# Kernel tuning notes

Measured on AMD Instinct MI355X. Metric: run time of the kernel, lower is better.

## Reference

```python
import jax, jax.numpy as jnp
import numpy as np
from jax import lax

SPARSITY = 0.5  # args.sparsity: fraction of weights KEPT


def get_subnet(scores, k):
    """GetSubnet.forward: sort |scores|, zero lowest (1-k) fraction, one elsewhere."""
    sa = jnp.abs(scores)
    n = sa.size
    j = int((1.0 - k) * n)  # static: number of entries zeroed
    idx = jnp.argsort(sa.ravel())  # ascending, matches torch .sort()
    mask = jnp.zeros((n,), dtype=sa.dtype).at[idx[j:]].set(1.0)
    return mask.reshape(scores.shape)


def masked_conv(x, w, s, b, stride):
    m = get_subnet(s, SPARSITY)
    y = lax.conv_general_dilated(
        x, w * m, window_strides=(stride, stride), padding=((1, 1), (1, 1)),
        dimension_numbers=('NCHW', 'OIHW', 'NCHW'))
    return y + b[None, :, None, None]


def setup_inputs() -> dict:
    key = jax.random.key(0)
    ks = jax.random.split(key, 16)
    def rn(k, shape, scale):
        return jax.random.normal(k, shape, dtype=jnp.float32) * scale
    return {
        'x':   rn(ks[0], (64, 3, 64, 64), 1.0),
        'w1':  rn(ks[1], (128, 3, 3, 3), 0.2),   's1': rn(ks[2], (128, 3, 3, 3), 1.0),   'b1': rn(ks[3], (128,), 0.01),
        'w2':  rn(ks[4], (256, 128, 3, 3), 0.05), 's2': rn(ks[5], (256, 128, 3, 3), 1.0), 'b2': rn(ks[6], (256,), 0.01),
        'w3':  rn(ks[7], (512, 256, 3, 3), 0.03), 's3': rn(ks[8], (512, 256, 3, 3), 1.0), 'b3': rn(ks[9], (512,), 0.01),
        'fw1': rn(ks[10], (1024, 512), 0.05),     'fs1': rn(ks[11], (1024, 512), 1.0),    'fb1': rn(ks[12], (1024,), 0.01),
        'fw2': rn(ks[13], (10, 1024), 0.05),      'fs2': rn(ks[14], (10, 1024), 1.0),     'fb2': rn(ks[15], (10,), 0.01),
    }


def reference(x, w1, s1, b1, w2, s2, b2, w3, s3, b3, fw1, fs1, fb1, fw2, fs2, fb2):
    h = jax.nn.relu(masked_conv(x, w1, s1, b1, stride=1))   # [64,128,64,64]
    h = jax.nn.relu(masked_conv(h, w2, s2, b2, stride=2))   # [64,256,32,32]
    h = jax.nn.relu(masked_conv(h, w3, s3, b3, stride=2))   # [64,512,16,16]
    h = h.mean(axis=(2, 3))                                 # [64,512] global avg pool
    m1 = get_subnet(fs1, SPARSITY)
    h = jax.nn.relu(h @ (fw1 * m1).T + fb1)                 # [64,1024]
    m2 = get_subnet(fs2, SPARSITY)
    return h @ (fw2 * m2).T + fb2                           # [64,10]
```

## Files before the change

### kernel.cpp

```cpp
#include <hip/hip_runtime.h>
#include <stdint.h>


typedef __attribute__((ext_vector_type(8))) short short8;
typedef __attribute__((ext_vector_type(4))) short short4v;
typedef __attribute__((ext_vector_type(4))) float floatx4;

__device__ __forceinline__ unsigned short f2bf(float f) {
    unsigned u = __float_as_uint(f);
    u += 0x7fffu + ((u >> 16) & 1u);
    return (unsigned short)(u >> 16);
}

__device__ __forceinline__ void stage16(const unsigned short* g, unsigned short* l) {
    __builtin_amdgcn_global_load_lds(
        (const __attribute__((address_space(1))) unsigned int*)(const void*)g,
        (__attribute__((address_space(3))) unsigned int*)(void*)l,
        16, 0, 0);
}

constexpr unsigned CUM0 = 3456u;
constexpr unsigned CUM1 = 298368u;
constexpr unsigned CUM2 = 1478016u;
constexpr unsigned CUM3 = 2002304u;
constexpr unsigned STOT = 2012544u;
constexpr int NBH = 512;

__device__ __forceinline__ int find_tensor(unsigned idx, unsigned& li) {
    if (idx < CUM0) { li = idx;        return 0; }
    if (idx < CUM1) { li = idx - CUM0; return 1; }
    if (idx < CUM2) { li = idx - CUM1; return 2; }
    if (idx < CUM3) { li = idx - CUM2; return 3; }
    li = idx - CUM3; return 4;
}

__global__ __launch_bounds__(256) void hist11(const float* __restrict__ s0,
                                              const float* __restrict__ s1,
                                              const float* __restrict__ s2,
                                              const float* __restrict__ s3,
                                              const float* __restrict__ s4,
                                              const unsigned* __restrict__ P,
                                              unsigned* __restrict__ ghist, int pass) {
    __shared__ unsigned lh[10240];
    const int tid = threadIdx.x;
    const int NB = (pass == 2) ? 512 : 2048;
    for (int i = tid; i < NB * 5; i += 256) lh[i] = 0;
    __syncthreads();

    unsigned pref[5];
    #pragma unroll
    for (int t = 0; t < 5; t++) pref[t] = pass ? P[t] : 0u;
    const int fsh = (pass == 1) ? 20 : 9;

    for (unsigned idx = blockIdx.x * 256u + tid; idx < STOT; idx += NBH * 256u) {
        unsigned li; int t = find_tensor(idx, li);
        const float* sp = t == 0 ? s0 : t == 1 ? s1 : t == 2 ? s2 : t == 3 ? s3 : s4;
        unsigned key = __float_as_uint(sp[li]) & 0x7fffffffu;
        bool ok = (pass == 0) || ((key >> fsh) == pref[t]);
        if (ok) {
            unsigned bin = (pass == 0) ? (key >> 20)
                         : (pass == 1) ? ((key >> 9) & 2047u)
                                       : (key & 511u);
            atomicAdd(&lh[(unsigned)t * NB + bin], 1u);
        }
    }
    __syncthreads();
    const int goff = (pass == 0) ? 0 : (pass == 1) ? 10240 : 20480;
    for (int i = tid; i < NB * 5; i += 256) {
        unsigned v = lh[i];
        if (v) atomicAdd(&ghist[goff + i], v);
    }
}

__global__ __launch_bounds__(256) void find11(const unsigned* __restrict__ ghist,
                                              unsigned* __restrict__ P,
                                              unsigned* __restrict__ targ, int pass) {
    const int t = blockIdx.x;
    const int tid = threadIdx.x;
    const int NB = (pass == 2) ? 512 : 2048;
    const int goff = (pass == 0) ? 0 : (pass == 1) ? 10240 : 20480;
    const int seg = NB / 256;
    __shared__ unsigned bins[2048];
    __shared__ unsigned part[256];
    for (int i = tid; i < NB; i += 256) bins[i] = ghist[goff + t * NB + i];
    __syncthreads();
    unsigned s = 0;
    for (int j = 0; j < seg; j++) s += bins[tid * seg + j];
    part[tid] = s;
    __syncthreads();
    if (tid == 0) {
        unsigned n = t == 0 ? 3456u : t == 1 ? 294912u : t == 2 ? 1179648u
                   : t == 3 ? 524288u : 10240u;
        unsigned target = (pass == 0) ? (n >> 1) : targ[t];
        unsigned cum = 0; int q = 0;
        for (; q < 256; q++) { unsigned c = part[q]; if (cum + c > target) break; cum += c; }
        int b = q * seg;
        for (;; b++) { unsigned c = bins[b]; if (cum + c > target) break; cum += c; }
        targ[t] = target - cum;
        if (pass == 0)      P[t] = (unsigned)b;
        else if (pass == 1) P[t] = (P[t] << 11) | (unsigned)b;
        else                P[t] = (P[t] << 9) | (unsigned)b;
    }
}

__global__ void mask_reorder(const float* __restrict__ w0, const float* __restrict__ w1,
                             const float* __restrict__ w2, const float* __restrict__ w3,
                             const float* __restrict__ w4,
                             const float* __restrict__ s0, const float* __restrict__ s1,
                             const float* __restrict__ s2, const float* __restrict__ s3,
                             const float* __restrict__ s4,
                             const unsigned* __restrict__ T,
                             float* __restrict__ wm1,
                             unsigned short* __restrict__ A2,
                             unsigned short* __restrict__ A3,
                             float* __restrict__ fwm1, float* __restrict__ fwm2,
                             float* __restrict__ pooled) {
    unsigned idx = blockIdx.x * 256u + threadIdx.x;
    if (idx >= STOT) return;
    if (idx < 32768u) pooled[idx] = 0.f;
    unsigned li; int t = find_tensor(idx, li);
    const float* sp = t == 0 ? s0 : t == 1 ? s1 : t == 2 ? s2 : t == 3 ? s3 : s4;
    const float* wp = t == 0 ? w0 : t == 1 ? w1 : t == 2 ? w2 : t == 3 ? w3 : w4;
    unsigned key = __float_as_uint(sp[li]) & 0x7fffffffu;
    float val = (key >= T[t]) ? wp[li] : 0.f;
    if (t == 0) {
        wm1[li] = val;
    } else if (t == 1) {
        unsigned k = li / 1152u, r = li - k * 1152u;
        unsigned c = r / 9u, e = r - c * 9u;
        A2[((size_t)e * 256u + k) * 128u + c] = f2bf(val);
    } else if (t == 2) {
        unsigned k = li / 2304u, r = li - k * 2304u;
        unsigned c = r / 9u, e = r - c * 9u;
        A3[((size_t)e * 512u + k) * 256u + c] = f2bf(val);
    } else if (t == 3) {
        fwm1[li] = val;
    } else {
        fwm2[li] = val;
    }
}

template <int C, int H, int W, int K, int TX, int TY, int KT>
__global__ __launch_bounds__(TX* TY) void conv_direct(const float* __restrict__ in,
                                                      const float* __restrict__ wm,
                                                      const float* __restrict__ bias,
                                                      unsigned short* __restrict__ out) {
    constexpr int TILW = TX * 2, TILH = TY * 2;
    constexpr int ITW = TILW + 2, ITH = TILH + 2;
    constexpr int NTHREADS = TX * TY;
    constexpr int NLOAD = (ITH * ITW + NTHREADS - 1) / NTHREADS;
    constexpr int KG = K / KT;

    __shared__ float sIn[ITH * ITW];
    __shared__ float sW[9 * KT];

    const int tid = threadIdx.x;
    const int tx = tid % TX, ty = tid / TX;
    const int kg = blockIdx.z % KG, n = blockIdx.z / KG;
    const int ox0 = blockIdx.x * TILW, oy0 = blockIdx.y * TILH;
    const int ix0 = ox0 - 1, iy0 = oy0 - 1;

    const float* inN = in + (size_t)n * C * H * W;
    const float* wkg = wm + (size_t)kg * KT * C * 9;

    int goff[NLOAD];
    #pragma unroll
    for (int i = 0; i < NLOAD; i++) {
        int idx = tid + i * NTHREADS;
        if (idx < ITH * ITW) {
            int r = idx / ITW, col = idx % ITW;
            int gy = iy0 + r, gx = ix0 + col;
            goff[i] = (gy >= 0 && gy < H && gx >= 0 && gx < W) ? (gy * W + gx) : -1;
        } else goff[i] = -2;
    }

    float acc[2][2][KT];
    #pragma unroll
    for (int py = 0; py < 2; py++)
        #pragma unroll
        for (int px = 0; px < 2; px++)
            #pragma unroll
            for (int j = 0; j < KT; j++) acc[py][px][j] = 0.f;

    for (int c = 0; c < C; c++) {
        const float* inC = inN + (size_t)c * H * W;
        #pragma unroll
        for (int i = 0; i < NLOAD; i++) {
            int g = goff[i];
            if (g >= -1) sIn[tid + i * NTHREADS] = (g >= 0) ? inC[g] : 0.f;
        }
        for (int i = tid; i < 9 * KT; i += NTHREADS) {
            int e = i / KT, j = i % KT;
            sW[i] = wkg[j * C * 9 + c * 9 + e];
        }
        __syncthreads();

        float vin[4][4];
        const float* base = &sIn[(ty * 2) * ITW + tx * 2];
        #pragma unroll
        for (int r = 0; r < 4; r++)
            #pragma unroll
            for (int cc = 0; cc < 4; cc++) vin[r][cc] = base[r * ITW + cc];

        #pragma unroll
        for (int e = 0; e < 9; e++) {
            const int dy = e / 3, dx = e % 3;
            #pragma unroll
            for (int j = 0; j < KT; j++) {
                float wv = sW[e * KT + j];
                #pragma unroll
                for (int py = 0; py < 2; py++)
                    #pragma unroll
                    for (int px = 0; px < 2; px++)
                        acc[py][px][j] = fmaf(vin[py + dy][px + dx], wv, acc[py][px][j]);
            }
        }
        __syncthreads();
    }

    float bj[KT];
    #pragma unroll
    for (int j = 0; j < KT; j++) bj[j] = bias[kg * KT + j];
    #pragma unroll
    for (int py = 0; py < 2; py++)
        #pragma unroll
        for (int px = 0; px < 2; px++) {
            int oy = oy0 + ty * 2 + py, ox = ox0 + tx * 2 + px;
            short8 v;
            #pragma unroll
            for (int j = 0; j < KT; j++) {
                float t = acc[py][px][j] + bj[j];
                v[j] = (short)f2bf(t > 0.f ? t : 0.f);
            }
            *(short8*)(out + ((size_t)(n * H + oy) * W + ox) * K + kg * KT) = v;
        }
}

template <int C, int H, int W, int KOUT, int NPIX, bool POOL, bool SWAPYZ>
__global__ __launch_bounds__(256, 3) void conv_mfma(const unsigned short* __restrict__ in,
                                                    const unsigned short* __restrict__ A,
                                                    const float* __restrict__ bias,
                                                    const unsigned short* __restrict__ zg,
                                                    void* __restrict__ outv) {
    constexpr int OH = H / 2, OW = W / 2;
    constexpr int PR = NPIX / OW;
    constexpr int FN = NPIX / 16;
    constexpr int RH = 2 * PR + 1;
    constexpr int IW = W + 1;
    constexpr int NC = C / 32;
    constexpr int NPT = RH * IW;
    constexpr int NPTP = (NPT + 7) & ~7;
    constexpr int NSLOT = 4 * NPTP;
    constexpr int SLMAX = (NSLOT + 255) / 256;
    constexpr int SLOTS_PAD = SLMAX * 256;

    __shared__ unsigned short sIn[2][SLOTS_PAD * 8];

    const int tid = threadIdx.x;
    const int lane = tid & 63;
    const int wv = tid >> 6;
    const int l15 = lane & 15;
    const int quad = lane >> 4;
    const int pt = blockIdx.x;
    const int kb = SWAPYZ ? blockIdx.z : blockIdx.y;
    const int n  = SWAPYZ ? blockIdx.y : blockIdx.z;
    const int k0 = kb * 128;
    const int oy0 = pt * PR;
    const int g0y = 2 * oy0 - 1;
    const int mw = wv * 32;

    int goff[SLMAX];
    #pragma unroll
    for (int i = 0; i < SLMAX; i++) {
        int s = tid + i * 256;
        int q = s / NPTP;
        int pix = s - q * NPTP;
        int pl = pix ^ ((pix >> 3) & 7);
        int iy = pl / IW, ix = pl - iy * IW;
        int gy = g0y + iy, gx = ix - 1;
        bool ok = (q < 4) && (pl < NPT) && (gy >= 0) && (gy < H) && (gx >= 0);
        goff[i] = ok ? ((gy * W + gx) * C + q * 8) : -1;
    }

    int pL[FN];
    #pragma unroll
    for (int fn = 0; fn < FN; fn++) {
        int p = fn * 16 + l15;
        int oyl = p / OW, oxl = p % OW;
        pL[fn] = oyl * 2 * IW + oxl * 2;
    }

    const unsigned short* inN = in + (size_t)n * H * W * C;

    floatx4 acc[2][FN];
    #pragma unroll
    for (int fm = 0; fm < 2; fm++)
        #pragma unroll
        for (int fn = 0; fn < FN; fn++) acc[fm][fn] = (floatx4){0.f, 0.f, 0.f, 0.f};

    auto stage_chunk = [&](unsigned short* sbuf, int cc) {
        const int cof = cc * 32;
        #pragma unroll
        for (int i = 0; i < SLMAX; i++) {
            const unsigned short* src = (goff[i] >= 0) ? (inN + goff[i] + cof) : zg;
            stage16(src, sbuf + (size_t)(tid + i * 256) * 8);
        }
    };

    const size_t estr = (size_t)KOUT * C;

    stage_chunk(&sIn[0][0], 0);

    #pragma unroll 1
    for (int cc = 0; cc < NC; cc++) {
        const int cur = cc & 1;
        const unsigned short* sb = &sIn[cur][0];

        if (cc + 1 < NC) {
            stage_chunk(&sIn[cur ^ 1][0], cc + 1);
            asm volatile("s_waitcnt vmcnt(%0)" :: "n"(SLMAX) : "memory");
        } else {
            asm volatile("s_waitcnt vmcnt(0)" ::: "memory");
        }
        __builtin_amdgcn_s_barrier();
        __builtin_amdgcn_sched_barrier(0);

        const unsigned short* Abase = A + (size_t)(k0 + mw + l15) * C + cc * 32 + quad * 8;
        short8 af[9][2];
        #pragma unroll
        for (int e = 0; e < 9; e++) {
            af[e][0] = *(const short8*)(Abase + (size_t)e * estr);
            af[e][1] = *(const short8*)(Abase + (size_t)e * estr + 16 * C);
        }

        #pragma unroll
        for (int e = 0; e < 9; e++) {
            const int dy = e / 3, dx = e - dy * 3;
            const int tof = dy * IW + dx;
            short8 bfr[FN];
            #pragma unroll
            for (int fn = 0; fn < FN; fn++) {
                int p = pL[fn] + tof;
                int pl = p ^ ((p >> 3) & 7);
                bfr[fn] = *(const short8*)(sb + ((size_t)quad * NPTP + pl) * 8);
            }
            #pragma unroll
            for (int fn = 0; fn < FN; fn++) {
                acc[0][fn] = __builtin_amdgcn_mfma_f32_16x16x32_bf16(af[e][0], bfr[fn], acc[0][fn], 0, 0, 0);
                acc[1][fn] = __builtin_amdgcn_mfma_f32_16x16x32_bf16(af[e][1], bfr[fn], acc[1][fn], 0, 0, 0);
            }
        }
        __builtin_amdgcn_s_barrier();
    }

    if (!POOL) {
        unsigned short* out = (unsigned short*)outv;
        #pragma unroll
        for (int fm = 0; fm < 2; fm++) {
            const int k4 = k0 + mw + fm * 16 + quad * 4;
            float b0 = bias[k4], b1 = bias[k4 + 1], b2 = bias[k4 + 2], b3 = bias[k4 + 3];
            #pragma unroll
            for (int fn = 0; fn < FN; fn++) {
                int p = fn * 16 + l15;
                int oy = oy0 + p / OW, ox = p % OW;
                float v0 = acc[fm][fn][0] + b0, v1 = acc[fm][fn][1] + b1;
                float v2 = acc[fm][fn][2] + b2, v3 = acc[fm][fn][3] + b3;
                short4v v;
                v[0] = (short)f2bf(v0 > 0.f ? v0 : 0.f);
                v[1] = (short)f2bf(v1 > 0.f ? v1 : 0.f);
                v[2] = (short)f2bf(v2 > 0.f ? v2 : 0.f);
                v[3] = (short)f2bf(v3 > 0.f ? v3 : 0.f);
                *(short4v*)(out + ((size_t)(n * OH + oy) * OW + ox) * KOUT + k4) = v;
            }
        }
    } else {
        float* out = (float*)outv;
        #pragma unroll
        for (int fm = 0; fm < 2; fm++) {
            #pragma unroll
            for (int reg = 0; reg < 4; reg++) {
                int k = k0 + mw + fm * 16 + quad * 4 + reg;
                float bv = bias[k];
                float s = 0.f;
                #pragma unroll
                for (int fn = 0; fn < FN; fn++) {
                    float v = acc[fm][fn][reg] + bv;
                    s += v > 0.f ? v : 0.f;
                }
                s += __shfl_xor(s, 1); s += __shfl_xor(s, 2);
                s += __shfl_xor(s, 4); s += __shfl_xor(s, 8);
                if (l15 == 0) atomicAdd(&out[n * KOUT + k], s * (1.0f / (OH * OW)));
            }
        }
    }
}

__global__ void fc1_kernel(const float* __restrict__ pooled, const float* __restrict__ w,
                           const float* __restrict__ b, float* __restrict__ out) {
    int t = blockIdx.x * 256 + threadIdx.x;
    int o = t & 1023, n = t >> 10;
    const float4* w4 = (const float4*)(w + (size_t)o * 512);
    const float4* p4 = (const float4*)(pooled + (size_t)n * 512);
    float acc = 0.f;
    for (int i = 0; i < 128; i++) {
        float4 a = p4[i], ww = w4[i];
        acc += a.x * ww.x + a.y * ww.y + a.z * ww.z + a.w * ww.w;
    }
    acc += b[o];
    out[t] = acc > 0.f ? acc : 0.f;
}

__global__ void fc2_kernel(const float* __restrict__ h, const float* __restrict__ w,
                           const float* __restrict__ b, float* __restrict__ out) {
    int n = blockIdx.x, tid = threadIdx.x;
    __shared__ float redw[40];
    const float4* h4 = (const float4*)(h + (size_t)n * 1024);
    float4 a = h4[tid];
    for (int o = 0; o < 10; o++) {
        const float4* w4 = (const float4*)(w + (size_t)o * 1024);
        float4 ww = w4[tid];
        float v = a.x * ww.x + a.y * ww.y + a.z * ww.z + a.w * ww.w;
        for (int off = 32; off > 0; off >>= 1) v += __shfl_down(v, off);
        if ((tid & 63) == 0) redw[o * 4 + (tid >> 6)] = v;
    }
    __syncthreads();
    if (tid < 10) {
        float s = redw[tid * 4] + redw[tid * 4 + 1] + redw[tid * 4 + 2] + redw[tid * 4 + 3] + b[tid];
        out[n * 10 + tid] = s;
    }
}

extern "C" void kernel_launch(void* const* d_in, const int* in_sizes, int n_in,
                              void* d_out, int out_size, void* d_ws, size_t ws_size,
                              hipStream_t stream) {
    const float* x   = (const float*)d_in[0];
    const float* w1  = (const float*)d_in[1];
    const float* s1  = (const float*)d_in[2];
    const float* b1  = (const float*)d_in[3];
    const float* w2  = (const float*)d_in[4];
    const float* s2  = (const float*)d_in[5];
    const float* b2  = (const float*)d_in[6];
    const float* w3  = (const float*)d_in[7];
    const float* s3  = (const float*)d_in[8];
    const float* b3  = (const float*)d_in[9];
    const float* fw1 = (const float*)d_in[10];
    const float* fs1 = (const float*)d_in[11];
    const float* fb1 = (const float*)d_in[12];
    const float* fw2 = (const float*)d_in[13];
    const float* fs2 = (const float*)d_in[14];
    const float* fb2 = (const float*)d_in[15];
    float* out = (float*)d_out;

    char* ws = (char*)d_ws;
    size_t off = 0;
    auto alloc = [&](size_t bytes) -> char* {
        char* p = ws + off;
        off = (off + bytes + 255) & ~(size_t)255;
        return p;
    };
    unsigned* ghist = (unsigned*)alloc(23040ull * 4);
    unsigned short* zguard = (unsigned short*)alloc(256);
    unsigned* P     = (unsigned*)alloc(64);
    unsigned* targ  = (unsigned*)alloc(64);
    float* wm1  = (float*)alloc(3456ull * 4);
    float* fwm1 = (float*)alloc(524288ull * 4);
    float* fwm2 = (float*)alloc(10240ull * 4);
    unsigned short* A2 = (unsigned short*)alloc(294912ull * 2);
    unsigned short* A3 = (unsigned short*)alloc(1179648ull * 2);
    unsigned short* h1 = (unsigned short*)alloc(33554432ull * 2);
    unsigned short* h2 = (unsigned short*)alloc(16777216ull * 2);
    float* pooled = (float*)alloc(32768ull * 4);
    float* fc1h   = (float*)alloc(65536ull * 4);
    if (off > ws_size) return;

    (void)hipMemsetAsync(ghist, 0, 23040ull * 4 + 256, stream);

    for (int pass = 0; pass < 3; pass++) {
        hist11<<<NBH, 256, 0, stream>>>(s1, s2, s3, fs1, fs2, P, ghist, pass);
        find11<<<5, 256, 0, stream>>>(ghist, P, targ, pass);
    }
    int gs = (STOT + 255) / 256;
    mask_reorder<<<gs, 256, 0, stream>>>(w1, w2, w3, fw1, fw2, s1, s2, s3, fs1, fs2, P,
                                         wm1, A2, A3, fwm1, fwm2, pooled);

    conv_direct<3, 64, 64, 128, 16, 16, 8>
        <<<dim3(2, 2, 64 * 16), 256, 0, stream>>>(x, wm1, b1, h1);
    conv_mfma<128, 64, 64, 256, 64, false, false>
        <<<dim3(16, 2, 64), 256, 0, stream>>>(h1, A2, b2, zguard, h2);
    conv_mfma<256, 32, 32, 512, 64, true, true>
        <<<dim3(4, 64, 4), 256, 0, stream>>>(h2, A3, b3, zguard, pooled);

    fc1_kernel<<<256, 256, 0, stream>>>(pooled, fwm1, fb1, fc1h);
    fc2_kernel<<<64, 256, 0, stream>>>(fc1h, fwm2, fb2, out);
}
```

Baseline: 448.1 us.

## Use pixel-major padded LDS layout and stream weight fragments per tap in conv

Changes the LDS staging layout of the input tile from quad-major with an XOR swizzle to pixel-major with a 5-slot (40-element) padded stride per pixel, avoiding bank conflicts without swizzle arithmetic. Weight fragments are now loaded one tap ahead inside a non-unrolled tap loop instead of preloading all nine taps, which cuts register pressure. The prefetch wait moves to the end of each chunk, and launch bounds drop from 3 to 2 blocks per CU. The padded layout uses more LDS slots and lowers occupancy, and the rolled tap loop may expose global-load latency on the weights.

```diff
diff --git a/kernel.cpp b/kernel.cpp
--- a/kernel.cpp
+++ b/kernel.cpp
@@ -237,7 +237,7 @@
 }
 
 template <int C, int H, int W, int KOUT, int NPIX, bool POOL, bool SWAPYZ>
-__global__ __launch_bounds__(256, 3) void conv_mfma(const unsigned short* __restrict__ in,
+__global__ __launch_bounds__(256, 2) void conv_mfma(const unsigned short* __restrict__ in,
                                                     const unsigned short* __restrict__ A,
                                                     const float* __restrict__ bias,
                                                     const unsigned short* __restrict__ zg,
@@ -249,12 +249,11 @@
     constexpr int IW = W + 1;
     constexpr int NC = C / 32;
     constexpr int NPT = RH * IW;
-    constexpr int NPTP = (NPT + 7) & ~7;
-    constexpr int NSLOT = 4 * NPTP;
+    constexpr int NSLOT = NPT * 5;
     constexpr int SLMAX = (NSLOT + 255) / 256;
-    constexpr int SLOTS_PAD = SLMAX * 256;
-
-    __shared__ unsigned short sIn[2][SLOTS_PAD * 8];
+    constexpr int SLOTS = SLMAX * 256;
+
+    __shared__ unsigned short sIn[2][SLOTS * 8];
 
     const int tid = threadIdx.x;
     const int lane = tid & 63;
@@ -273,21 +272,19 @@
     #pragma unroll
     for (int i = 0; i < SLMAX; i++) {
         int s = tid + i * 256;
-        int q = s / NPTP;
-        int pix = s - q * NPTP;
-        int pl = pix ^ ((pix >> 3) & 7);
-        int iy = pl / IW, ix = pl - iy * IW;
+        int pix = s / 5, q = s - pix * 5;
+        int iy = pix / IW, ix = pix - iy * IW;
         int gy = g0y + iy, gx = ix - 1;
-        bool ok = (q < 4) && (pl < NPT) && (gy >= 0) && (gy < H) && (gx >= 0);
+        bool ok = (s < NSLOT) && (q < 4) && (gy >= 0) && (gy < H) && (gx >= 0);
         goff[i] = ok ? ((gy * W + gx) * C + q * 8) : -1;
     }
 
-    int pL[FN];
+    int pB[FN];
     #pragma unroll
     for (int fn = 0; fn < FN; fn++) {
         int p = fn * 16 + l15;
         int oyl = p / OW, oxl = p % OW;
-        pL[fn] = oyl * 2 * IW + oxl * 2;
+        pB[fn] = (oyl * 2 * IW + oxl * 2) * 40 + quad * 8;
     }
 
     const unsigned short* inN = in + (size_t)n * H * W * C;
@@ -298,59 +295,57 @@
         #pragma unroll
         for (int fn = 0; fn < FN; fn++) acc[fm][fn] = (floatx4){0.f, 0.f, 0.f, 0.f};
 
-    auto stage_chunk = [&](unsigned short* sbuf, int cc) {
+    const size_t estr = (size_t)KOUT * C;
+    const int wvb = tid & 192;
+
+    auto stage_chunk = [&](int buf, int cc) {
         const int cof = cc * 32;
         #pragma unroll
         for (int i = 0; i < SLMAX; i++) {
             const unsigned short* src = (goff[i] >= 0) ? (inN + goff[i] + cof) : zg;
-            stage16(src, sbuf + (size_t)(tid + i * 256) * 8);
+            stage16(src, &sIn[buf][(size_t)(i * 256 + wvb) * 8]);
         }
     };
 
-    const size_t estr = (size_t)KOUT * C;
-
-    stage_chunk(&sIn[0][0], 0);
+    stage_chunk(0, 0);
+    asm volatile("s_waitcnt vmcnt(0)" ::: "memory");
+    __builtin_amdgcn_s_barrier();
+    __builtin_amdgcn_sched_barrier(0);
 
     #pragma unroll 1
     for (int cc = 0; cc < NC; cc++) {
         const int cur = cc & 1;
         const unsigned short* sb = &sIn[cur][0];
 
-        if (cc + 1 < NC) {
-            stage_chunk(&sIn[cur ^ 1][0], cc + 1);
-            asm volatile("s_waitcnt vmcnt(%0)" :: "n"(SLMAX) : "memory");
-        } else {
-            asm volatile("s_waitcnt vmcnt(0)" ::: "memory");
-        }
+        if (cc + 1 < NC) stage_chunk(cur ^ 1, cc + 1);
+
+        const unsigned short* Abase = A + (size_t)(k0 + mw + l15) * C + cc * 32 + quad * 8;
+        short8 a0 = *(const short8*)(Abase);
+        short8 a1 = *(const short8*)(Abase + 16 * C);
+
+        #pragma unroll 1
+        for (int e = 0; e < 9; e++) {
+            short8 ac0 = a0, ac1 = a1;
+            if (e < 8) {
+                a0 = *(const short8*)(Abase + (size_t)(e + 1) * estr);
+                a1 = *(const short8*)(Abase + (size_t)(e + 1) * estr + 16 * C);
+            }
+            const int dy = e / 3, dx = e - dy * 3;
+            const int boff = (dy * IW + dx) * 40;
+            short8 bfr[FN];
+            #pragma unroll
+            for (int fn = 0; fn < FN; fn++)
+                bfr[fn] = *(const short8*)(sb + pB[fn] + boff);
+            #pragma unroll
+            for (int fn = 0; fn < FN; fn++) {
+                acc[0][fn] = __builtin_amdgcn_mfma_f32_16x16x32_bf16(ac0, bfr[fn], acc[0][fn], 0, 0, 0);
+                acc[1][fn] = __builtin_amdgcn_mfma_f32_16x16x32_bf16(ac1, bfr[fn], acc[1][fn], 0, 0, 0);
+            }
+        }
+
+        asm volatile("s_waitcnt vmcnt(0)" ::: "memory");
         __builtin_amdgcn_s_barrier();
         __builtin_amdgcn_sched_barrier(0);
-
-        const unsigned short* Abase = A + (size_t)(k0 + mw + l15) * C + cc * 32 + quad * 8;
-        short8 af[9][2];
-        #pragma unroll
-        for (int e = 0; e < 9; e++) {
-            af[e][0] = *(const short8*)(Abase + (size_t)e * estr);
-            af[e][1] = *(const short8*)(Abase + (size_t)e * estr + 16 * C);
-        }
-
-        #pragma unroll
-        for (int e = 0; e < 9; e++) {
-            const int dy = e / 3, dx = e - dy * 3;
-            const int tof = dy * IW + dx;
-            short8 bfr[FN];
-            #pragma unroll
-            for (int fn = 0; fn < FN; fn++) {
-                int p = pL[fn] + tof;
-                int pl = p ^ ((p >> 3) & 7);
-                bfr[fn] = *(const short8*)(sb + ((size_t)quad * NPTP + pl) * 8);
-            }
-            #pragma unroll
-            for (int fn = 0; fn < FN; fn++) {
-                acc[0][fn] = __builtin_amdgcn_mfma_f32_16x16x32_bf16(af[e][0], bfr[fn], acc[0][fn], 0, 0, 0);
-                acc[1][fn] = __builtin_amdgcn_mfma_f32_16x16x32_bf16(af[e][1], bfr[fn], acc[1][fn], 0, 0, 0);
-            }
-        }
-        __builtin_amdgcn_s_barrier();
     }
 
     if (!POOL) {
```

New measurement: 444.3 us. About the same (-0.9%).
